# Kernel optimization log

Hardware: AMD Instinct MI355X
Metric: run time of the kernel (lower is better)

The kernel has to match this reference:

```python
import jax, jax.numpy as jnp
import numpy as np

C_NUM, D_NUM = 64, 128
N_NODES = C_NUM * D_NUM + C_NUM + D_NUM  # 8384
HEADS, OUT = 4, 256


def gat_conv(h, src, dst, W, al, ar, b):
    """DGL-style GATConv (eval mode, attn_drop off). h:[N,F], W:[F,H*O], al/ar:[H,O], b:[H*O]."""
    N = h.shape[0]
    H, O = al.shape
    feat = (h @ W).reshape(N, H, O)
    el = jnp.sum(feat * al, axis=-1)                      # [N,H]
    er = jnp.sum(feat * ar, axis=-1)
    e = jax.nn.leaky_relu(el[src] + er[dst], 0.2)         # [E,H]
    m = jax.ops.segment_max(e, dst, num_segments=N)
    m = jnp.where(jnp.isfinite(m), m, 0.0)
    p = jnp.exp(e - m[dst])
    s = jax.ops.segment_sum(p, dst, num_segments=N)
    a = p / jnp.maximum(s[dst], 1e-9)                     # edge softmax per dst, per head
    out = jax.ops.segment_sum(a[:, :, None] * feat[src], dst, num_segments=N)  # [N,H,O]
    return out + b.reshape(1, H, O)


def cagat_layer(edges, dfeat, cvec, gw, al, ar, gb,
                wq_w, wq_b, wk_w, wk_b, wv_w, wv_b, ip_w, ip_b, op_w, op_b):
    ch = cvec.shape[1]
    pad = jnp.repeat(cvec, D_NUM, axis=0)                       # [c*d, ch]
    pad3 = jnp.broadcast_to(cvec.mean(axis=0), (D_NUM, ch))      # [d, ch]
    cfin = jnp.concatenate([pad, cvec, pad3], axis=0)            # [N, ch]
    inf = jnp.concatenate([dfeat, cfin], axis=1)                 # [N, F+ch]
    # 4 relation-specific GATConvs, stacked (HeteroGraphConv aggregate='stack')
    rst = jnp.stack([gat_conv(inf, edges[t, 0], edges[t, 1], gw[t], al[t], ar[t], gb[t])
                     for t in range(4)], axis=1)                 # [N,4,H,O]
    N = inf.shape[0]
    rst = rst.reshape(N, 4 * HEADS, OUT)
    E = OUT
    Q = (cfin @ wq_w + wq_b)[:, None, :]                         # [N,1,E]
    K = rst @ wk_w + wk_b                                        # [N,16,E]
    V = rst @ wv_w + wv_b
    # nn.MultiheadAttention(E, 1): in-proj then single-head SDPA then out-proj
    q = Q @ ip_w[:E].T + ip_b[:E]
    k = K @ ip_w[E:2 * E].T + ip_b[E:2 * E]
    v = V @ ip_w[2 * E:].T + ip_b[2 * E:]
    att = jax.nn.softmax(jnp.einsum('nqe,nke->nqk', q, k) / jnp.sqrt(jnp.float32(E)), axis=-1)
    o = jnp.einsum('nqk,nke->nqe', att, v) @ op_w.T + op_b
    return o.reshape(N, E)


def setup_inputs() -> dict:
    key = jax.random.key(0)
    ks = iter(jax.random.split(key, 64))
    rn = lambda shape: jax.random.normal(next(ks), shape, jnp.float32) * 0.05
    inp = {}
    inp['x'] = rn((D_NUM, 256))
    inp['cf'] = rn((C_NUM, 512))
    inp['cf_net_w'] = rn((512, 128)); inp['cf_net_b'] = rn((128,))
    inp['ht_w'] = rn((512, 256)); inp['ht_b'] = rn((256,))
    for l in ('1', '2'):
        inp['gw' + l] = rn((4, 384, HEADS * OUT))
        inp['al' + l] = rn((4, HEADS, OUT))
        inp['ar' + l] = rn((4, HEADS, OUT))
        inp['gb' + l] = rn((4, HEADS * OUT))
        inp['wq' + l + '_w'] = rn((128, 256)); inp['wq' + l + '_b'] = rn((256,))
        inp['wk' + l + '_w'] = rn((256, 256)); inp['wk' + l + '_b'] = rn((256,))
        inp['wv' + l + '_w'] = rn((256, 256)); inp['wv' + l + '_b'] = rn((256,))
        inp['ip' + l + '_w'] = rn((768, 256)); inp['ip' + l + '_b'] = rn((768,))
        inp['op' + l + '_w'] = rn((256, 256)); inp['op' + l + '_b'] = rn((256,))
    inp['edges'] = jax.random.randint(next(ks), (4, 2, 50000), 0, N_NODES, dtype=jnp.int32)
    return inp


def reference(x, cf, cf_net_w, cf_net_b, ht_w, ht_b,
              gw1, al1, ar1, gb1, wq1_w, wq1_b, wk1_w, wk1_b, wv1_w, wv1_b, ip1_w, ip1_b, op1_w, op1_b,
              gw2, al2, ar2, gb2, wq2_w, wq2_b, wk2_w, wk2_b, wv2_w, wv2_b, ip2_w, ip2_b, op2_w, op2_b,
              edges):
    cf_vec = cf @ cf_net_w + cf_net_b                           # [c, cell_hidden]
    d_pad = jnp.tile(x, (C_NUM, 1))                             # [c*d, in]
    d_uc = cf @ ht_w + ht_b                                     # [c, in]
    d_feat = jnp.concatenate([d_pad, d_uc, x], axis=0)          # [N, in]
    h = cagat_layer(edges, d_feat, cf_vec, gw1, al1, ar1, gb1,
                    wq1_w, wq1_b, wk1_w, wk1_b, wv1_w, wv1_b, ip1_w, ip1_b, op1_w, op1_b)
    h = cagat_layer(edges, h, cf_vec, gw2, al2, ar2, gb2,
                    wq2_w, wq2_b, wk2_w, wk2_b, wv2_w, wv2_b, ip2_w, ip2_b, op2_w, op2_b)
    return h
```

## Files before the change

kernel.cpp:

```cpp
#include <hip/hip_runtime.h>
#include <hip/hip_bf16.h>

typedef __hip_bfloat16 bf16;
typedef __attribute__((ext_vector_type(8))) short short8;
typedef __attribute__((ext_vector_type(4))) short short4v;
typedef __attribute__((ext_vector_type(4))) float f32x4;

#define KN 8384
#define KNPAD 8448
#define KE 50000
#define NBIG 4480

__device__ __forceinline__ float toF(float v){ return v; }
__device__ __forceinline__ float toF(bf16 v){ return __bfloat162float(v); }
__device__ __forceinline__ float b2f(short u){ return __uint_as_float(((unsigned int)(unsigned short)u) << 16); }
__device__ __forceinline__ void stor(float* p, float v){ *p = v; }
__device__ __forceinline__ void stor(bf16* p, float v){ *p = __float2bfloat16(v); }

__device__ __forceinline__ void glds16(const bf16* g, bf16* l){
  __builtin_amdgcn_global_load_lds(
      (const __attribute__((address_space(1))) unsigned int*)(g),
      (__attribute__((address_space(3))) unsigned int*)(l), 16, 0, 0);
}

template<typename TC>
__global__ __launch_bounds__(256)
void gemm_mfma_bt(const bf16* __restrict__ A, const bf16* __restrict__ BT,
                  const float* __restrict__ bias, TC* __restrict__ C,
                  int M, int N, int K, int ldc, int nbx)
{
  __shared__ bf16 As[3][128 * 32];
  __shared__ bf16 Bs[3][128 * 32];
  const int nwg = gridDim.x;
  const int q = nwg >> 3, r = nwg & 7;
  const int xcd = blockIdx.x & 7, idx = blockIdx.x >> 3;
  const int sw = (xcd < r) ? xcd * (q + 1) + idx : r * (q + 1) + (xcd - r) * q + idx;
  const int bn = (sw % nbx) * 128, bm = (sw / nbx) * 128;
  const int tid = threadIdx.x;
  const int w = tid >> 6, l = tid & 63;
  const int wr = (w >> 1) * 64, wc = (w & 1) * 64;
  const int lr = l & 15;
  int rS[2], lqS[2];
  #pragma unroll
  for (int i = 0; i < 2; i++){
    rS[i] = w * 32 + i * 16 + (l >> 2);
    lqS[i] = (l & 3) ^ ((rS[i] >> 1) & 3);
  }
  const bf16* gA0 = A  + (size_t)(bm + rS[0]) * K + lqS[0] * 8;
  const bf16* gA1 = A  + (size_t)(bm + rS[1]) * K + lqS[1] * 8;
  const bf16* gB0 = BT + (size_t)(bn + rS[0]) * K + lqS[0] * 8;
  const bf16* gB1 = BT + (size_t)(bn + rS[1]) * K + lqS[1] * 8;
  const int nt = K >> 5;
  auto issue = [&](int t){
    int b = t - (t / 3) * 3;
    int k0 = t << 5;
    glds16(gA0 + k0, &As[b][w * 1024]);
    glds16(gA1 + k0, &As[b][w * 1024 + 512]);
    glds16(gB0 + k0, &Bs[b][w * 1024]);
    glds16(gB1 + k0, &Bs[b][w * 1024 + 512]);
  };
  f32x4 acc[4][4] = {};
  issue(0);
  issue(1);
  for (int t = 0; t < nt; t++){
    if (t < nt - 1) asm volatile("s_waitcnt vmcnt(4)\ns_barrier" ::: "memory");
    else            asm volatile("s_waitcnt vmcnt(0)\ns_barrier" ::: "memory");
    if (t + 2 < nt) issue(t + 2);
    int b = t - (t / 3) * 3;
    short8 a[4], bb[4];
    #pragma unroll
    for (int i = 0; i < 4; i++){
      int R = wr + i * 16 + lr;
      int pq = (l >> 4) ^ ((R >> 1) & 3);
      a[i] = *(short8*)&As[b][R * 32 + pq * 8];
    }
    #pragma unroll
    for (int j = 0; j < 4; j++){
      int R = wc + j * 16 + lr;
      int pq = (l >> 4) ^ ((R >> 1) & 3);
      bb[j] = *(short8*)&Bs[b][R * 32 + pq * 8];
    }
    #pragma unroll
    for (int i = 0; i < 4; i++)
      #pragma unroll
      for (int j = 0; j < 4; j++)
        acc[i][j] = __builtin_amdgcn_mfma_f32_16x16x32_bf16(a[i], bb[j], acc[i][j], 0, 0, 0);
  }
  const int orow = (l >> 4) * 4, ocol = l & 15;
  #pragma unroll
  for (int i = 0; i < 4; i++){
    #pragma unroll
    for (int j = 0; j < 4; j++){
      int gcol = bn + wc + j * 16 + ocol;
      float bv = bias ? bias[gcol] : 0.f;
      #pragma unroll
      for (int rg = 0; rg < 4; rg++){
        int grow = bm + wr + i * 16 + orow + rg;
        if (grow < M) stor(&C[(size_t)grow * ldc + gcol], acc[i][j][rg] + bv);
      }
    }
  }
}

struct LPtrs {
  const float *gw[2], *al[2], *ar[2];
  const float *wqw[2], *wqb[2], *wkw[2], *wvw[2], *wvb[2];
  const float *ipw[2], *ipb[2], *opw[2], *opb[2];
  bf16* bigBT[2];
  float *ipwQT[2], *wkwT[2], *opwT[2], *wvwT[2];
  float *Wq[2], *B2[2], *M1[2], *bq[2];
  bf16* WvT[2];
  float *bv[2], *biasc[2];
  int* cnt;
};

#define PT0 1536
#define PT1 4608
#define PT2 4864
#define PT3 5248
#define PT4 5392
#define PT5 5524
__global__ __launch_bounds__(256)
void k_prep_all(LPtrs P){
  const int lay = blockIdx.z;
  const int b = blockIdx.x, tid = threadIdx.x;
  bf16* bigBT = P.bigBT[lay];
  if (b < PT0){
    __shared__ float t[32][33];
    int rel = b / 384, rem = b % 384;
    int n0 = (rem % 32) * 32, k0 = (rem / 32) * 32;
    const float* B = P.gw[lay] + (size_t)rel * 384 * 1024;
    bf16* BT = bigBT + (size_t)rel * 1024 * 384;
    int tx = tid & 31, ty = tid >> 5;
    for (int i = ty; i < 32; i += 8)
      t[i][tx] = B[(size_t)(k0 + i) * 1024 + n0 + tx];
    __syncthreads();
    for (int i = ty; i < 32; i += 8)
      BT[(size_t)(n0 + i) * 384 + k0 + tx] = __float2bfloat16(t[tx][i]);
  } else if (b < PT1){
    int bb = b - PT0;
    int kblk = bb % 96, r = bb / 96;
    int k = kblk * 4 + (tid >> 6), lane = tid & 63;
    int rr = r & 15, t = rr >> 2, h = rr & 3;
    const float* wsrc = ((r < 16) ? P.al[lay] : P.ar[lay]) + t * 1024 + h * 256;
    const float* gp = P.gw[lay] + (size_t)t * 384 * 1024 + (size_t)k * 1024 + h * 256;
    float v = 0.f;
    #pragma unroll
    for (int i = 0; i < 4; i++){
      int o = lane + i * 64;
      v += gp[o] * wsrc[o];
    }
    #pragma unroll
    for (int off = 32; off; off >>= 1) v += __shfl_down(v, off);
    if (lane == 0) bigBT[(size_t)(4352 + r) * 384 + k] = __float2bfloat16(v);
  } else if (b < PT2){
    __shared__ float t[32][33];
    int bb = b - PT1;
    int mat = bb >> 6, rem = bb & 63;
    int c0 = (rem & 7) * 32, r0 = (rem >> 3) * 32;
    const float* S; float* D;
    switch (mat){
      case 0: S = P.ipw[lay]; D = P.ipwQT[lay]; break;
      case 1: S = P.wkw[lay]; D = P.wkwT[lay]; break;
      case 2: S = P.opw[lay]; D = P.opwT[lay]; break;
      default: S = P.wvw[lay]; D = P.wvwT[lay]; break;
    }
    int tx = tid & 31, ty = tid >> 5;
    for (int i = ty; i < 32; i += 8)
      t[i][tx] = S[(size_t)(r0 + i) * 256 + c0 + tx];
    __syncthreads();
    for (int i = ty; i < 32; i += 8)
      D[(size_t)(c0 + i) * 256 + r0 + tx] = t[tx][i];
  } else if (b < PT3){
    int idx = (b - PT2) * 256 + tid;
    bigBT[(size_t)(4096 + idx / 384) * 384 + idx % 384] = __float2bfloat16(0.f);
  } else if (b < PT4){
    int idx = (b - PT3) * 256 + tid;
    bigBT[(size_t)(4384 + idx / 384) * 384 + idx % 384] = __float2bfloat16(0.f);
  } else if (lay == 0){
    int idx = (b - PT4) * 256 + tid;
    if (idx < 4 * KN) P.cnt[idx] = 0;
  }
}

__global__ __launch_bounds__(256)
void k_fold1(LPtrs P){
  const int lay = blockIdx.z;
  int b = blockIdx.x, tid = threadIdx.x;
  if (b < 128){
    int c = b; float s = 0.f;
    for (int e = 0; e < 256; e++) s += P.wqw[lay][c * 256 + e] * P.ipwQT[lay][e * 256 + tid];
    P.Wq[lay][c * 256 + tid] = s;
  } else if (b < 384){
    int j = b - 128; float s = 0.f;
    for (int e = 0; e < 256; e++) s += P.wkwT[lay][e * 256 + tid] * P.ipw[lay][(256 + j) * 256 + e];
    P.B2[lay][j * 256 + tid] = s;
  } else if (b < 640){
    int e = b - 384; float s = 0.f;
    for (int f = 0; f < 256; f++) s += P.ipw[lay][(512 + f) * 256 + e] * P.opwT[lay][f * 256 + tid];
    P.M1[lay][e * 256 + tid] = s;
  } else {
    float s = 0.f;
    for (int e = 0; e < 256; e++) s += P.wqb[lay][e] * P.ipwQT[lay][e * 256 + tid];
    P.bq[lay][tid] = s + P.ipb[lay][tid];
  }
}

__global__ __launch_bounds__(256)
void k_fold2(LPtrs P){
  const int lay = blockIdx.z;
  int b = blockIdx.x, tid = threadIdx.x;
  if (b < 256){
    __shared__ float wqr[256];
    wqr[tid] = P.Wq[lay][b * 256 + tid];
    __syncthreads();
    float s = 0.f;
    for (int j = 0; j < 256; j++) s += wqr[j] * P.B2[lay][j * 256 + tid];
    P.bigBT[lay][(size_t)(4096 + tid) * 384 + 256 + b] = __float2bfloat16(s);
  } else if (b < 512){
    int j = b - 256; float s = 0.f;
    for (int e = 0; e < 256; e++) s += P.wvwT[lay][e * 256 + tid] * P.M1[lay][e * 256 + j];
    P.WvT[lay][j * 256 + tid] = __float2bfloat16(s);
  } else {
    float b2 = 0.f;
    for (int j = 0; j < 256; j++) b2 += P.bq[lay][j] * P.B2[lay][j * 256 + tid];
    float s = 0.f;
    for (int e = 0; e < 256; e++) s += P.wvb[lay][e] * P.M1[lay][e * 256 + tid];
    for (int f = 0; f < 256; f++) s += P.ipb[lay][512 + f] * P.opwT[lay][f * 256 + tid];
    P.bv[lay][tid] = s + P.opb[lay][tid];
    for (int i = tid; i < NBIG; i += 256)
      P.biasc[lay][i] = (i - 4096 == tid) ? b2 : 0.f;
  }
}

__global__ __launch_bounds__(384)
void k_pre(const float* __restrict__ cf, const float* __restrict__ cfw, const float* __restrict__ cfb,
           const float* __restrict__ htw, const float* __restrict__ htb,
           float* __restrict__ cfvec, float* __restrict__ duc)
{
  int c = blockIdx.x;
  int col = threadIdx.x;
  __shared__ float row[512];
  for (int i = col; i < 512; i += 384) row[i] = cf[c * 512 + i];
  __syncthreads();
  if (col < 128){
    float acc = cfb[col];
    for (int k = 0; k < 512; k++) acc += row[k] * cfw[k * 128 + col];
    cfvec[c * 128 + col] = acc;
  } else {
    int j = col - 128;
    float acc = htb[j];
    for (int k = 0; k < 512; k++) acc += row[k] * htw[k * 256 + j];
    duc[c * 256 + j] = acc;
  }
}
__global__ void k_mean(const float* cv, float* m){
  int o = threadIdx.x;
  float s = 0.f;
  for (int c = 0; c < 64; c++) s += cv[c * 128 + o];
  m[o] = s * (1.f / 64.f);
}
__global__ __launch_bounds__(384)
void k_infasm(const float* __restrict__ x, const float* __restrict__ duc,
              const float* __restrict__ cv, const float* __restrict__ cm,
              bf16* __restrict__ inf){
  int n = blockIdx.x, o = threadIdx.x;
  float v;
  if (o < 256){
    if (n < 8192)      v = x[(n & 127) * 256 + o];
    else if (n < 8256) v = duc[(n - 8192) * 256 + o];
    else               v = x[(n - 8256) * 256 + o];
  } else {
    int oo = o - 256;
    if (n < 8192)      v = cv[(n >> 7) * 128 + oo];
    else if (n < 8256) v = cv[(n - 8192) * 128 + oo];
    else               v = cm[oo];
  }
  inf[(size_t)n * 384 + o] = __float2bfloat16(v);
}
__global__ __launch_bounds__(384)
void k_smallA(const float* __restrict__ x, const float* __restrict__ cv,
              bf16* __restrict__ A12){
  int r = blockIdx.x, c = threadIdx.x;
  float v = 0.f;
  if (r < 128){
    if (c < 256) v = x[r * 256 + c];
  } else if (r < 192){
    if (c >= 256) v = cv[(r - 128) * 128 + (c - 256)];
  }
  A12[(size_t)r * 384 + c] = __float2bfloat16(v);
}
__global__ void k_countB(const int* __restrict__ edges, int* __restrict__ cnt){
  int i = blockIdx.x * blockDim.x + threadIdx.x;
  if (i < 4 * KE){
    int t = i / KE, idx = i - t * KE;
    int d = edges[t * 2 * KE + KE + idx];
    atomicAdd(&cnt[t * KN + d], 1);
  }
}
__global__ void k_fillB(const int* __restrict__ edges, int* __restrict__ cur, int* __restrict__ csrc){
  int i = blockIdx.x * blockDim.x + threadIdx.x;
  if (i < 4 * KE){
    int t = i / KE, idx = i - t * KE;
    int s = edges[t * 2 * KE + idx];
    int d = edges[t * 2 * KE + KE + idx];
    int p = atomicAdd(&cur[t * KN + d], 1);
    csrc[p] = s;
  }
}
__global__ void k_scan(const int* __restrict__ cnt, int* __restrict__ ptr,
                       int* __restrict__ cur, int n){
  __shared__ int part[1024];
  int tid = threadIdx.x;
  const int CH = (n + 1023) >> 10;
  int base = tid * CH;
  int s = 0;
  for (int i = 0; i < CH; i++){ int idx = base + i; if (idx < n) s += cnt[idx]; }
  part[tid] = s; __syncthreads();
  for (int off = 1; off < 1024; off <<= 1){
    int v = (tid >= off) ? part[tid - off] : 0;
    __syncthreads();
    part[tid] += v;
    __syncthreads();
  }
  int run = part[tid] - s;
  for (int i = 0; i < CH; i++){
    int idx = base + i;
    if (idx < n){ ptr[idx] = run; cur[idx] = run; run += cnt[idx]; }
  }
  if (tid == 1023) ptr[n] = part[1023];
}

template<int LR>
__global__ __launch_bounds__(256)
void k_aggattn(const int* __restrict__ ptr, const int* __restrict__ csrc,
               const bf16* __restrict__ big, const bf16* __restrict__ T12,
               const float* __restrict__ biasc, const float* __restrict__ gb,
               bf16* __restrict__ rbar)
{
  const int n = blockIdx.x, tid = threadIdx.x;
  const int w = tid >> 6, lane = tid & 63;
  const int t = w;
  const int head = lane >> 4;
  __shared__ float s_rst[16][260];
  __shared__ float s_sc[16];
  __shared__ float sa4[4][64][4];
  __shared__ int ssrcW[4][64];
  const int beg = ptr[t * KN + n], deg = ptr[t * KN + n + 1] - beg;
  auto elr4 = [&](int node, int base, float* out){
    if (LR && node < 8192){
      short4v u = *(const short4v*)&T12[(size_t)(node & 127) * NBIG + base + t * 4];
      short4v v = *(const short4v*)&T12[(size_t)(128 + (node >> 7)) * NBIG + base + t * 4];
      #pragma unroll
      for (int h = 0; h < 4; h++) out[h] = b2f(u[h]) + b2f(v[h]);
    } else {
      short4v u = *(const short4v*)&big[(size_t)node * NBIG + base + t * 4];
      #pragma unroll
      for (int h = 0; h < 4; h++) out[h] = b2f(u[h]);
    }
  };
  float ern[4];
  elr4(n, 4368, ern);
  float sums[4] = {0.f, 0.f, 0.f, 0.f};
  for (int j = lane; j < deg; j += 64){
    int s = csrc[beg + j];
    float el4[4];
    elr4(s, 4352, el4);
    #pragma unroll
    for (int h = 0; h < 4; h++){
      float e = el4[h] + ern[h];
      e = e > 0.f ? e : 0.2f * e;
      sums[h] += __expf(e);
    }
  }
  #pragma unroll
  for (int off = 32; off; off >>= 1){
    #pragma unroll
    for (int h = 0; h < 4; h++) sums[h] += __shfl_xor(sums[h], off);
  }
  float sinv[4];
  #pragma unroll
  for (int h = 0; h < 4; h++) sinv[h] = 1.f / fmaxf(sums[h], 1e-9f);
  float acc[16];
  #pragma unroll
  for (int i = 0; i < 16; i++) acc[i] = 0.f;
  const size_t cbase = (size_t)t * 1024 + lane * 16;
  for (int c0 = 0; c0 < deg; c0 += 64){
    int cn = min(64, deg - c0);
    if (lane < cn){
      int s = csrc[beg + c0 + lane];
      ssrcW[t][lane] = s;
      float el4[4];
      elr4(s, 4352, el4);
      #pragma unroll
      for (int h = 0; h < 4; h++){
        float e = el4[h] + ern[h];
        e = e > 0.f ? e : 0.2f * e;
        sa4[t][lane][h] = __expf(e) * sinv[h];
      }
    }
    if (LR){
      for (int j = 0; j < cn; j++){
        int s = ssrcW[t][j];
        float wj = sa4[t][j][head];
        if (s < 8192){
          const bf16* p1 = &T12[(size_t)(s & 127) * NBIG + cbase];
          const bf16* p2 = &T12[(size_t)(128 + (s >> 7)) * NBIG + cbase];
          short8 u0 = *(const short8*)p1, u1 = *(const short8*)(p1 + 8);
          short8 v0 = *(const short8*)p2, v1 = *(const short8*)(p2 + 8);
          #pragma unroll
          for (int i = 0; i < 8; i++) acc[i] += wj * (b2f(u0[i]) + b2f(v0[i]));
          #pragma unroll
          for (int i = 0; i < 8; i++) acc[8 + i] += wj * (b2f(u1[i]) + b2f(v1[i]));
        } else {
          const bf16* fp = &big[(size_t)s * NBIG + cbase];
          short8 v0 = *(const short8*)fp, v1 = *(const short8*)(fp + 8);
          #pragma unroll
          for (int i = 0; i < 8; i++) acc[i] += wj * b2f(v0[i]);
          #pragma unroll
          for (int i = 0; i < 8; i++) acc[8 + i] += wj * b2f(v1[i]);
        }
      }
    } else {
      int j = 0;
      for (; j + 3 < cn; j += 4){
        int s0 = ssrcW[t][j],     s1 = ssrcW[t][j + 1];
        int s2 = ssrcW[t][j + 2], s3 = ssrcW[t][j + 3];
        float w0 = sa4[t][j][head],     w1 = sa4[t][j + 1][head];
        float w2 = sa4[t][j + 2][head], w3 = sa4[t][j + 3][head];
        const bf16* f0 = &big[(size_t)s0 * NBIG + cbase];
        const bf16* f1 = &big[(size_t)s1 * NBIG + cbase];
        const bf16* f2 = &big[(size_t)s2 * NBIG + cbase];
        const bf16* f3 = &big[(size_t)s3 * NBIG + cbase];
        short8 a0 = *(const short8*)f0, b0 = *(const short8*)(f0 + 8);
        short8 a1 = *(const short8*)f1, b1 = *(const short8*)(f1 + 8);
        short8 a2 = *(const short8*)f2, b2 = *(const short8*)(f2 + 8);
        short8 a3 = *(const short8*)f3, b3 = *(const short8*)(f3 + 8);
        #pragma unroll
        for (int i = 0; i < 8; i++)
          acc[i] += w0 * b2f(a0[i]) + w1 * b2f(a1[i]) + w2 * b2f(a2[i]) + w3 * b2f(a3[i]);
        #pragma unroll
        for (int i = 0; i < 8; i++)
          acc[8 + i] += w0 * b2f(b0[i]) + w1 * b2f(b1[i]) + w2 * b2f(b2[i]) + w3 * b2f(b3[i]);
      }
      for (; j < cn; j++){
        int s = ssrcW[t][j];
        float wj = sa4[t][j][head];
        const bf16* fp = &big[(size_t)s * NBIG + cbase];
        short8 v0 = *(const short8*)fp;
        short8 v1 = *(const short8*)(fp + 8);
        #pragma unroll
        for (int i = 0; i < 8; i++) acc[i] += wj * b2f(v0[i]);
        #pragma unroll
        for (int i = 0; i < 8; i++) acc[8 + i] += wj * b2f(v1[i]);
      }
    }
  }
  {
    const float* gbp = gb + t * 1024 + lane * 16;
    float* rp = &s_rst[t * 4 + head][(lane & 15) * 16];
    #pragma unroll
    for (int i = 0; i < 16; i++) rp[i] = acc[i] + gbp[i];
  }
  __syncthreads();
  #pragma unroll
  for (int si = 0; si < 4; si++){
    int s = w * 4 + si;
    float v = 0.f;
    #pragma unroll
    for (int i = 0; i < 4; i++){
      int o = lane + i * 64;
      float qo;
      if (LR && n < 8192)
        qo = b2f(T12[(size_t)(n & 127) * NBIG + 4096 + o]) +
             b2f(T12[(size_t)(128 + (n >> 7)) * NBIG + 4096 + o]) + biasc[4096 + o];
      else
        qo = toF(big[(size_t)n * NBIG + 4096 + o]);
      v += s_rst[s][o] * qo;
    }
    #pragma unroll
    for (int off = 32; off; off >>= 1) v += __shfl_down(v, off);
    if (lane == 0) s_sc[s] = v * 0.0625f;
  }
  __syncthreads();
  float sc[16]; float m = -1e30f;
  #pragma unroll
  for (int s = 0; s < 16; s++){ sc[s] = s_sc[s]; m = fmaxf(m, sc[s]); }
  float sum = 0.f;
  #pragma unroll
  for (int s = 0; s < 16; s++){ sc[s] = __expf(sc[s] - m); sum += sc[s]; }
  float inv = 1.f / sum;
  float r = 0.f;
  #pragma unroll
  for (int s = 0; s < 16; s++) r += sc[s] * s_rst[s][tid];
  rbar[(size_t)n * 256 + tid] = __float2bfloat16(r * inv);
}

extern "C" void kernel_launch(void* const* d_in, const int* in_sizes, int n_in,
                              void* d_out, int out_size, void* d_ws, size_t ws_size,
                              hipStream_t stream)
{
  const float* x   = (const float*)d_in[0];
  const float* cf  = (const float*)d_in[1];
  const float* cfw = (const float*)d_in[2];
  const float* cfb = (const float*)d_in[3];
  const float* htw = (const float*)d_in[4];
  const float* htb = (const float*)d_in[5];
  LPtrs P;
  const float* gbp[2];
  for (int l = 0; l < 2; l++){
    int b = 6 + l * 14;
    P.gw[l]  = (const float*)d_in[b + 0];
    P.al[l]  = (const float*)d_in[b + 1];
    P.ar[l]  = (const float*)d_in[b + 2];
    gbp[l]   = (const float*)d_in[b + 3];
    P.wqw[l] = (const float*)d_in[b + 4];
    P.wqb[l] = (const float*)d_in[b + 5];
    P.wkw[l] = (const float*)d_in[b + 6];
    P.wvw[l] = (const float*)d_in[b + 8];
    P.wvb[l] = (const float*)d_in[b + 9];
    P.ipw[l] = (const float*)d_in[b + 10];
    P.ipb[l] = (const float*)d_in[b + 11];
    P.opw[l] = (const float*)d_in[b + 12];
    P.opb[l] = (const float*)d_in[b + 13];
  }
  const int* edges = (const int*)d_in[34];

  char* w = (char*)d_ws;
  size_t off = 0;
  auto alc = [&](size_t bytes) -> void* {
    off = (off + 255) & ~(size_t)255;
    void* p = w + off; off += bytes; return p;
  };
  float* f_cfvec = (float*)alc(64 * 128 * 4);
  float* f_cfmean= (float*)alc(128 * 4);
  float* f_duc   = (float*)alc(64 * 256 * 4);
  bf16*  b_inf   = (bf16*) alc((size_t)KNPAD * 384 * 2);
  bf16*  b_big   = (bf16*) alc((size_t)KN * NBIG * 2);
  bf16*  b_rbar  = (bf16*) alc((size_t)KNPAD * 256 * 2);
  bf16*  b_A12   = (bf16*) alc((size_t)256 * 384 * 2);
  bf16*  b_T12   = (bf16*) alc((size_t)192 * NBIG * 2);
  for (int l = 0; l < 2; l++){
    P.bigBT[l] = (bf16*) alc((size_t)NBIG * 384 * 2);
    P.biasc[l] = (float*)alc((size_t)NBIG * 4);
    P.ipwQT[l] = (float*)alc(256 * 256 * 4);
    P.wkwT[l]  = (float*)alc(256 * 256 * 4);
    P.opwT[l]  = (float*)alc(256 * 256 * 4);
    P.wvwT[l]  = (float*)alc(256 * 256 * 4);
    P.Wq[l]    = (float*)alc(128 * 256 * 4);
    P.B2[l]    = (float*)alc(256 * 256 * 4);
    P.M1[l]    = (float*)alc(256 * 256 * 4);
    P.bq[l]    = (float*)alc(256 * 4);
    P.bv[l]    = (float*)alc(256 * 4);
    P.WvT[l]   = (bf16*) alc(256 * 256 * 2);
  }
  int* i_ptr = (int*)alc((size_t)(4 * KN + 1) * 4);
  int* i_src = (int*)alc((size_t)4 * KE * 4);
  int* i_cnt = (int*)alc((size_t)4 * KN * 4);
  int* i_cur = (int*)alc((size_t)4 * KN * 4);
  P.cnt = i_cnt;
  if (off > ws_size) return;

  k_pre<<<64, 384, 0, stream>>>(cf, cfw, cfb, htw, htb, f_cfvec, f_duc);
  k_mean<<<1, 128, 0, stream>>>(f_cfvec, f_cfmean);
  k_infasm<<<KN, 384, 0, stream>>>(x, f_duc, f_cfvec, f_cfmean, b_inf);
  k_smallA<<<256, 384, 0, stream>>>(x, f_cfvec, b_A12);
  k_prep_all<<<dim3(PT5, 1, 2), 256, 0, stream>>>(P);
  k_fold1<<<dim3(641, 1, 2), 256, 0, stream>>>(P);
  k_fold2<<<dim3(513, 1, 2), 256, 0, stream>>>(P);

  k_countB<<<(4 * KE + 255) / 256, 256, 0, stream>>>(edges, i_cnt);
  k_scan<<<1, 1024, 0, stream>>>(i_cnt, i_ptr, i_cur, 4 * KN);
  k_fillB<<<(4 * KE + 255) / 256, 256, 0, stream>>>(edges, i_cur, i_src);

  gemm_mfma_bt<bf16><<<(NBIG / 128) * 2, 256, 0, stream>>>(
      b_A12, P.bigBT[0], nullptr, b_T12, 192, NBIG, 384, NBIG, NBIG / 128);
  gemm_mfma_bt<bf16><<<(NBIG / 128) * 2, 256, 0, stream>>>(
      b_inf + (size_t)8192 * 384, P.bigBT[0], P.biasc[0],
      b_big + (size_t)8192 * NBIG, 192, NBIG, 384, NBIG, NBIG / 128);
  k_aggattn<1><<<KN, 256, 0, stream>>>(i_ptr, i_src, b_big, b_T12, P.biasc[0], gbp[0], b_rbar);
  gemm_mfma_bt<bf16><<<2 * 66, 256, 0, stream>>>(
      b_rbar, P.WvT[0], P.bv[0], b_inf, KN, 256, 256, 384, 2);

  gemm_mfma_bt<bf16><<<(NBIG / 128) * 66, 256, 0, stream>>>(
      b_inf, P.bigBT[1], P.biasc[1], b_big, KN, NBIG, 384, NBIG, NBIG / 128);
  k_aggattn<0><<<KN, 256, 0, stream>>>(i_ptr, i_src, b_big, b_T12, P.biasc[1], gbp[1], b_rbar);
  gemm_mfma_bt<float><<<2 * 66, 256, 0, stream>>>(
      b_rbar, P.WvT[1], P.bv[1], (float*)d_out, KN, 256, 256, 256, 2);
}
```

Before: 492.3 us.

## Materialize layer-1 factored features into dense buffer before aggregation

Adds a kernel that expands the low-rank T12 factors (x-row part plus cell part) into the full per-node feature buffer for the first 8192 nodes. The layer-1 aggregation can then use the same 4-way unrolled gather as layer 2 instead of a branchy path that does two loads per edge. The input assembly kernel is split so only the cell-feature columns are written for every node and the x/duc columns only for the tail strip, since the head rows of those columns are no longer read. In exchange it adds a write of about 8192×4480 bf16 (~73MB) plus a read of T12, trading extra bandwidth for a simpler, more parallel gather.

Measured after the change: 517.7 us. 1.05x slower.

```diff
diff --git a/kernel.cpp b/kernel.cpp
--- a/kernel.cpp
+++ b/kernel.cpp
@@ -260,22 +260,19 @@
   for (int c = 0; c < 64; c++) s += cv[c * 128 + o];
   m[o] = s * (1.f / 64.f);
 }
-__global__ __launch_bounds__(384)
-void k_infasm(const float* __restrict__ x, const float* __restrict__ duc,
-              const float* __restrict__ cv, const float* __restrict__ cm,
-              bf16* __restrict__ inf){
-  int n = blockIdx.x, o = threadIdx.x;
+__global__ void k_cfincol(const float* __restrict__ cv, const float* __restrict__ cm,
+                          bf16* __restrict__ inf){
+  int n = blockIdx.x, oo = threadIdx.x;
   float v;
-  if (o < 256){
-    if (n < 8192)      v = x[(n & 127) * 256 + o];
-    else if (n < 8256) v = duc[(n - 8192) * 256 + o];
-    else               v = x[(n - 8256) * 256 + o];
-  } else {
-    int oo = o - 256;
-    if (n < 8192)      v = cv[(n >> 7) * 128 + oo];
-    else if (n < 8256) v = cv[(n - 8192) * 128 + oo];
-    else               v = cm[oo];
-  }
+  if (n < 8192)      v = cv[(n >> 7) * 128 + oo];
+  else if (n < 8256) v = cv[(n - 8192) * 128 + oo];
+  else               v = cm[oo];
+  inf[(size_t)n * 384 + 256 + oo] = __float2bfloat16(v);
+}
+__global__ void k_infstrip(const float* __restrict__ x, const float* __restrict__ duc,
+                           bf16* __restrict__ inf){
+  int n = 8192 + blockIdx.x, o = threadIdx.x;
+  float v = (n < 8256) ? duc[(n - 8192) * 256 + o] : x[(n - 8256) * 256 + o];
   inf[(size_t)n * 384 + o] = __float2bfloat16(v);
 }
 __global__ __launch_bounds__(384)
@@ -289,6 +286,22 @@
     if (c >= 256) v = cv[(r - 128) * 128 + (c - 256)];
   }
   A12[(size_t)r * 384 + c] = __float2bfloat16(v);
+}
+__global__ __launch_bounds__(256)
+void k_expandF(const bf16* __restrict__ T12, bf16* __restrict__ big){
+  int n = blockIdx.x;
+  const bf16* t1 = T12 + (size_t)(n & 127) * NBIG;
+  const bf16* t2 = T12 + (size_t)(128 + (n >> 7)) * NBIG;
+  bf16* out = big + (size_t)n * NBIG;
+  #pragma unroll
+  for (int it = 0; it < 2; it++){
+    int c = threadIdx.x * 8 + it * 2048;
+    short8 u = *(const short8*)&t1[c];
+    short8 v = *(const short8*)&t2[c];
+    #pragma unroll
+    for (int i = 0; i < 8; i++)
+      out[c + i] = __float2bfloat16(b2f(u[i]) + b2f(v[i]));
+  }
 }
 __global__ void k_countB(const int* __restrict__ edges, int* __restrict__ cnt){
   int i = blockIdx.x * blockDim.x + threadIdx.x;
@@ -399,61 +412,37 @@
         sa4[t][lane][h] = __expf(e) * sinv[h];
       }
     }
-    if (LR){
-      for (int j = 0; j < cn; j++){
-        int s = ssrcW[t][j];
-        float wj = sa4[t][j][head];
-        if (s < 8192){
-          const bf16* p1 = &T12[(size_t)(s & 127) * NBIG + cbase];
-          const bf16* p2 = &T12[(size_t)(128 + (s >> 7)) * NBIG + cbase];
-          short8 u0 = *(const short8*)p1, u1 = *(const short8*)(p1 + 8);
-          short8 v0 = *(const short8*)p2, v1 = *(const short8*)(p2 + 8);
-          #pragma unroll
-          for (int i = 0; i < 8; i++) acc[i] += wj * (b2f(u0[i]) + b2f(v0[i]));
-          #pragma unroll
-          for (int i = 0; i < 8; i++) acc[8 + i] += wj * (b2f(u1[i]) + b2f(v1[i]));
-        } else {
-          const bf16* fp = &big[(size_t)s * NBIG + cbase];
-          short8 v0 = *(const short8*)fp, v1 = *(const short8*)(fp + 8);
-          #pragma unroll
-          for (int i = 0; i < 8; i++) acc[i] += wj * b2f(v0[i]);
-          #pragma unroll
-          for (int i = 0; i < 8; i++) acc[8 + i] += wj * b2f(v1[i]);
-        }
-      }
-    } else {
-      int j = 0;
-      for (; j + 3 < cn; j += 4){
-        int s0 = ssrcW[t][j],     s1 = ssrcW[t][j + 1];
-        int s2 = ssrcW[t][j + 2], s3 = ssrcW[t][j + 3];
-        float w0 = sa4[t][j][head],     w1 = sa4[t][j + 1][head];
-        float w2 = sa4[t][j + 2][head], w3 = sa4[t][j + 3][head];
-        const bf16* f0 = &big[(size_t)s0 * NBIG + cbase];
-        const bf16* f1 = &big[(size_t)s1 * NBIG + cbase];
-        const bf16* f2 = &big[(size_t)s2 * NBIG + cbase];
-        const bf16* f3 = &big[(size_t)s3 * NBIG + cbase];
-        short8 a0 = *(const short8*)f0, b0 = *(const short8*)(f0 + 8);
-        short8 a1 = *(const short8*)f1, b1 = *(const short8*)(f1 + 8);
-        short8 a2 = *(const short8*)f2, b2 = *(const short8*)(f2 + 8);
-        short8 a3 = *(const short8*)f3, b3 = *(const short8*)(f3 + 8);
-        #pragma unroll
-        for (int i = 0; i < 8; i++)
-          acc[i] += w0 * b2f(a0[i]) + w1 * b2f(a1[i]) + w2 * b2f(a2[i]) + w3 * b2f(a3[i]);
-        #pragma unroll
-        for (int i = 0; i < 8; i++)
-          acc[8 + i] += w0 * b2f(b0[i]) + w1 * b2f(b1[i]) + w2 * b2f(b2[i]) + w3 * b2f(b3[i]);
-      }
-      for (; j < cn; j++){
-        int s = ssrcW[t][j];
-        float wj = sa4[t][j][head];
-        const bf16* fp = &big[(size_t)s * NBIG + cbase];
-        short8 v0 = *(const short8*)fp;
-        short8 v1 = *(const short8*)(fp + 8);
-        #pragma unroll
-        for (int i = 0; i < 8; i++) acc[i] += wj * b2f(v0[i]);
-        #pragma unroll
-        for (int i = 0; i < 8; i++) acc[8 + i] += wj * b2f(v1[i]);
-      }
+    int j = 0;
+    for (; j + 3 < cn; j += 4){
+      int s0 = ssrcW[t][j],     s1 = ssrcW[t][j + 1];
+      int s2 = ssrcW[t][j + 2], s3 = ssrcW[t][j + 3];
+      float w0 = sa4[t][j][head],     w1 = sa4[t][j + 1][head];
+      float w2 = sa4[t][j + 2][head], w3 = sa4[t][j + 3][head];
+      const bf16* f0 = &big[(size_t)s0 * NBIG + cbase];
+      const bf16* f1 = &big[(size_t)s1 * NBIG + cbase];
+      const bf16* f2 = &big[(size_t)s2 * NBIG + cbase];
+      const bf16* f3 = &big[(size_t)s3 * NBIG + cbase];
+      short8 a0 = *(const short8*)f0, b0 = *(const short8*)(f0 + 8);
+      short8 a1 = *(const short8*)f1, b1 = *(const short8*)(f1 + 8);
+      short8 a2 = *(const short8*)f2, b2 = *(const short8*)(f2 + 8);
+      short8 a3 = *(const short8*)f3, b3 = *(const short8*)(f3 + 8);
+      #pragma unroll
+      for (int i = 0; i < 8; i++)
+        acc[i] += w0 * b2f(a0[i]) + w1 * b2f(a1[i]) + w2 * b2f(a2[i]) + w3 * b2f(a3[i]);
+      #pragma unroll
+      for (int i = 0; i < 8; i++)
+        acc[8 + i] += w0 * b2f(b0[i]) + w1 * b2f(b1[i]) + w2 * b2f(b2[i]) + w3 * b2f(b3[i]);
+    }
+    for (; j < cn; j++){
+      int s = ssrcW[t][j];
+      float wj = sa4[t][j][head];
+      const bf16* fp = &big[(size_t)s * NBIG + cbase];
+      short8 v0 = *(const short8*)fp;
+      short8 v1 = *(const short8*)(fp + 8);
+      #pragma unroll
+      for (int i = 0; i < 8; i++) acc[i] += wj * b2f(v0[i]);
+      #pragma unroll
+      for (int i = 0; i < 8; i++) acc[8 + i] += wj * b2f(v1[i]);
     }
   }
   {
@@ -563,7 +552,8 @@
 
   k_pre<<<64, 384, 0, stream>>>(cf, cfw, cfb, htw, htb, f_cfvec, f_duc);
   k_mean<<<1, 128, 0, stream>>>(f_cfvec, f_cfmean);
-  k_infasm<<<KN, 384, 0, stream>>>(x, f_duc, f_cfvec, f_cfmean, b_inf);
+  k_cfincol<<<KN, 128, 0, stream>>>(f_cfvec, f_cfmean, b_inf);
+  k_infstrip<<<192, 256, 0, stream>>>(x, f_duc, b_inf);
   k_smallA<<<256, 384, 0, stream>>>(x, f_cfvec, b_A12);
   k_prep_all<<<dim3(PT5, 1, 2), 256, 0, stream>>>(P);
   k_fold1<<<dim3(641, 1, 2), 256, 0, stream>>>(P);
@@ -578,6 +568,7 @@
   gemm_mfma_bt<bf16><<<(NBIG / 128) * 2, 256, 0, stream>>>(
       b_inf + (size_t)8192 * 384, P.bigBT[0], P.biasc[0],
       b_big + (size_t)8192 * NBIG, 192, NBIG, 384, NBIG, NBIG / 128);
+  k_expandF<<<8192, 256, 0, stream>>>(b_T12, b_big);
   k_aggattn<1><<<KN, 256, 0, stream>>>(i_ptr, i_src, b_big, b_T12, P.biasc[0], gbp[0], b_rbar);
   gemm_mfma_bt<bf16><<<2 * 66, 256, 0, stream>>>(
       b_rbar, P.WvT[0], P.bv[0], b_inf, KN, 256, 256, 384, 2);
```
